# Kernel tuning notes

Hardware: AMD Instinct MI355X
Metric: run time of the kernel (lower is better)

The kernel has to match this reference:

```python
import jax, jax.numpy as jnp
import numpy as np

BN_EPS = 1e-5


def setup_inputs() -> dict:
    key = jax.random.key(0)
    ks = jax.random.split(key, 4)
    B, N, D = 8, 8192, 256
    outD = 256
    s = 1.0 / np.sqrt(D)
    return {
        "feature": jax.random.normal(ks[0], (B, N, D), dtype=jnp.float32),
        "W_qk": jax.random.normal(ks[1], (2, D, D), dtype=jnp.float32) * s,
        "b_qk": jnp.zeros((2, D), dtype=jnp.float32),
        "W_v": jax.random.normal(ks[2], (D, outD), dtype=jnp.float32) * s,
        "b_v": jnp.zeros((outD,), dtype=jnp.float32),
        "gamma": jnp.ones((D,), dtype=jnp.float32),
        "beta": jnp.zeros((D,), dtype=jnp.float32),
    }


def reference(feature, W_qk, b_qk, W_v, b_v, gamma, beta):
    # QK: [B, 2, N, D]
    QK = jnp.einsum("bnd,kde->bkne", feature, W_qk) + b_qk[None, :, None, :]
    # value: [B, N, outD]
    value = jnp.einsum("bnd,de->bne", feature, W_v) + b_v
    query = QK[:, 0]  # [B, N, D]
    key = QK[:, 1]    # [B, N, D]
    # softmax over the sequence axis (dim=1), per (batch, channel)
    sm = jax.nn.softmax(key, axis=1)
    # lambda context: softmax^T @ value -> [B, D, outD]
    lam = jnp.einsum("bnd,bne->bde", sm, value)
    # BatchNorm1d(featureDim) in training mode: channel axis = D (axis 1),
    # stats over (batch, spatial) = axes (0, 2); biased variance as torch uses.
    mean = jnp.mean(lam, axis=(0, 2), keepdims=True)
    var = jnp.var(lam, axis=(0, 2), keepdims=True)
    bn = (lam - mean) * jax.lax.rsqrt(var + BN_EPS)
    bn = bn * gamma[None, :, None] + beta[None, :, None]
    # result: query @ BN -> [B, N, outD]
    return jnp.einsum("bnd,bde->bne", query, bn)
```

## Files before the change

### kernel.cpp

```cpp
#include <hip/hip_runtime.h>

typedef unsigned short u16;
typedef __bf16 bf16x8 __attribute__((ext_vector_type(8)));
typedef float f32x4 __attribute__((ext_vector_type(4)));

#define LOG2E 1.44269504088896f

__device__ inline u16 f2b(float f) {
    unsigned u = __float_as_uint(f);
    u += 0x7fff + ((u >> 16) & 1);
    return (u16)(u >> 16);
}
__device__ inline float b2f(u16 u) { return __uint_as_float(((unsigned)u) << 16); }
__device__ inline unsigned pk2(float a, float b) {
    return (unsigned)f2b(a) | ((unsigned)f2b(b) << 16);
}
__device__ inline uint4 pack8(float4 a, float4 b) {
    return uint4{pk2(a.x, a.y), pk2(a.z, a.w), pk2(b.x, b.y), pk2(b.z, b.w)};
}
__device__ inline f32x4 mfma_bf16(uint4 a, uint4 b, f32x4 c) {
    return __builtin_amdgcn_mfma_f32_16x16x32_bf16(
        __builtin_bit_cast(bf16x8, a), __builtin_bit_cast(bf16x8, b), c, 0, 0, 0);
}
__device__ inline void ld16(const u16* g, u16* l) {
    __builtin_amdgcn_global_load_lds(
        (const __attribute__((address_space(1))) unsigned int*)g,
        (__attribute__((address_space(3))) unsigned int*)l, 16, 0, 0);
}

__global__ __launch_bounds__(256) void prep_w(const float* __restrict__ Wqk,
                                              const float* __restrict__ Wv,
                                              u16* __restrict__ WkT,
                                              u16* __restrict__ WvT,
                                              u16* __restrict__ Wqb) {
    int idx = blockIdx.x * 256 + threadIdx.x;
    int which = idx >> 16;
    int i = (idx >> 8) & 255;
    int j = idx & 255;
    if (which == 0)
        WkT[i * 256 + j] = f2b(Wqk[65536 + j * 256 + i]);
    else if (which == 1)
        WvT[i * 256 + j] = f2b(Wv[j * 256 + i]);
    else
        Wqb[i * 256 + j] = f2b(Wqk[i * 256 + j]);
}

__global__ __launch_bounds__(256, 2) void gemm_kv(const float* __restrict__ A,
                                                  const u16* __restrict__ BtK,
                                                  const u16* __restrict__ BtV,
                                                  const float* __restrict__ biasK,
                                                  const float* __restrict__ biasV,
                                                  u16* __restrict__ KT,
                                                  u16* __restrict__ VT) {
    __shared__ __align__(16) u16 lds[18432];
    u16* As = lds;
    u16* BsK = lds + 2048;
    u16* BsV = lds + 10240;

    const int t = threadIdx.x;
    const int r0 = blockIdx.x * 64;
    const int w = t >> 6, lane = t & 63, l15 = lane & 15, q = lane >> 4;

    f32x4 accK[16], accV[16];
#pragma unroll
    for (int c = 0; c < 16; ++c) {
        accK[c] = f32x4{0.f, 0.f, 0.f, 0.f};
        accV[c] = f32x4{0.f, 0.f, 0.f, 0.f};
    }

    const int ar = t >> 2;
    const int ak = (t & 3) * 8;
    const float* Arow = A + (long)(r0 + ar) * 256 + ak;
    u16* AsW = As + t * 8;

    float4 a0 = ((const float4*)Arow)[0];
    float4 a1 = ((const float4*)Arow)[1];

    for (int k0 = 0; k0 < 256; k0 += 32) {
#pragma unroll
        for (int j = 0; j < 4; ++j) {
            int ch = j * 256 + t;
            int br = ch >> 2;
            int bk = (ch & 3) * 8;
            ld16(BtK + br * 256 + k0 + bk, BsK + j * 2048 + w * 512);
            ld16(BtV + br * 256 + k0 + bk, BsV + j * 2048 + w * 512);
        }
        *(uint4*)AsW = pack8(a0, a1);
        __syncthreads();
        if (k0 + 32 < 256) {
            a0 = ((const float4*)(Arow + k0 + 32))[0];
            a1 = ((const float4*)(Arow + k0 + 32))[1];
        }
        uint4 af = *(const uint4*)(As + (w * 16 + l15) * 32 + q * 8);
#pragma unroll
        for (int c = 0; c < 16; ++c) {
            uint4 bK = *(const uint4*)(BsK + (c * 16 + l15) * 32 + q * 8);
            uint4 bV = *(const uint4*)(BsV + (c * 16 + l15) * 32 + q * 8);
            accK[c] = mfma_bf16(af, bK, accK[c]);
            accV[c] = mfma_bf16(af, bV, accV[c]);
        }
        __syncthreads();
    }

    const int bb = r0 >> 13, n0 = r0 & 8191;
    u16* Ct = lds;
#pragma unroll
    for (int pass = 0; pass < 2; ++pass) {
        const f32x4* acc = pass ? accV : accK;
        const float* bias = pass ? biasV : biasK;
        u16* CT = pass ? VT : KT;
#pragma unroll
        for (int c = 0; c < 16; ++c) {
            float bv = bias[c * 16 + l15];
            ushort4 pk;
            pk.x = f2b(acc[c][0] + bv);
            pk.y = f2b(acc[c][1] + bv);
            pk.z = f2b(acc[c][2] + bv);
            pk.w = f2b(acc[c][3] + bv);
            *(ushort4*)&Ct[(c * 16 + l15) * 72 + w * 16 + q * 4] = pk;
        }
        __syncthreads();
        long off = ((long)bb * 256 + t) * 8192 + n0;
#pragma unroll
        for (int j = 0; j < 8; ++j)
            *(uint4*)(CT + off + j * 8) = *(const uint4*)&Ct[t * 72 + j * 8];
        __syncthreads();
    }
}

__global__ __launch_bounds__(256, 3) void gemm_out(const float* __restrict__ A,
                                                   const u16* __restrict__ WfoldT,
                                                   const float* __restrict__ outb,
                                                   float* __restrict__ C) {
    __shared__ __align__(16) u16 lds[10240];
    u16* As = lds;
    u16* Bs = lds + 2048;

    const int t = threadIdx.x;
    const int r0 = blockIdx.x * 64;
    const int bb = r0 >> 13;
    const int w = t >> 6, lane = t & 63, l15 = lane & 15, q = lane >> 4;
    const u16* Bt = WfoldT + (long)bb * 65536;

    f32x4 acc[16];
#pragma unroll
    for (int c = 0; c < 16; ++c) acc[c] = f32x4{0.f, 0.f, 0.f, 0.f};

    const float* Arow = A + (long)(r0 + (t >> 2)) * 256 + (t & 3) * 8;
    u16* AsW = As + t * 8;

    float4 a0 = ((const float4*)Arow)[0];
    float4 a1 = ((const float4*)Arow)[1];

    for (int k0 = 0; k0 < 256; k0 += 32) {
#pragma unroll
        for (int j = 0; j < 4; ++j) {
            int ch = j * 256 + t;
            ld16(Bt + (ch >> 2) * 256 + k0 + (ch & 3) * 8, Bs + j * 2048 + w * 512);
        }
        *(uint4*)AsW = pack8(a0, a1);
        __syncthreads();
        if (k0 + 32 < 256) {
            a0 = ((const float4*)(Arow + k0 + 32))[0];
            a1 = ((const float4*)(Arow + k0 + 32))[1];
        }
        uint4 af = *(const uint4*)(As + (w * 16 + l15) * 32 + q * 8);
#pragma unroll
        for (int c = 0; c < 16; ++c) {
            uint4 bf = *(const uint4*)(Bs + (c * 16 + l15) * 32 + q * 8);
            acc[c] = mfma_bf16(af, bf, acc[c]);
        }
        __syncthreads();
    }

#pragma unroll
    for (int c = 0; c < 16; ++c) {
        int col = c * 16 + l15;
        float bv = outb[bb * 256 + col];
#pragma unroll
        for (int r = 0; r < 4; ++r) {
            int row = r0 + w * 16 + q * 4 + r;
            C[(long)row * 256 + col] = acc[c][r] + bv;
        }
    }
}

__global__ __launch_bounds__(256, 4) void gemm_splitk(const u16* __restrict__ VT,
                                                      const u16* __restrict__ PT,
                                                      float* __restrict__ lamP,
                                                      int chunk) {
    __shared__ __align__(16) u16 lds[8192];
    u16* As = lds;
    u16* Bs = lds + 4096;

    const int t = threadIdx.x;
    const int r0 = blockIdx.x * 128;
    const int c0 = blockIdx.y * 128;
    const int s = blockIdx.z;
    const int bb = blockIdx.x >> 1;
    const long n0 = (long)s * chunk;
    const int w = t >> 6, lane = t & 63, l15 = lane & 15, q = lane >> 4;

    f32x4 acc[2][8];
#pragma unroll
    for (int rt = 0; rt < 2; ++rt)
#pragma unroll
        for (int c = 0; c < 8; ++c) acc[rt][c] = f32x4{0.f, 0.f, 0.f, 0.f};

    for (int k0 = 0; k0 < chunk; k0 += 32) {
#pragma unroll
        for (int j = 0; j < 2; ++j) {
            int ch = j * 256 + t;
            int br = ch >> 2;
            int bk = (ch & 3) * 8;
            ld16(VT + (long)(r0 + br) * 8192 + n0 + k0 + bk, As + j * 2048 + w * 512);
            ld16(PT + ((long)bb * 256 + c0 + br) * 8192 + n0 + k0 + bk,
                 Bs + j * 2048 + w * 512);
        }
        __syncthreads();
        uint4 af0 = *(const uint4*)(As + (w * 32 + l15) * 32 + q * 8);
        uint4 af1 = *(const uint4*)(As + (w * 32 + 16 + l15) * 32 + q * 8);
#pragma unroll
        for (int c = 0; c < 8; ++c) {
            uint4 bf = *(const uint4*)(Bs + (c * 16 + l15) * 32 + q * 8);
            acc[0][c] = mfma_bf16(af0, bf, acc[0][c]);
            acc[1][c] = mfma_bf16(af1, bf, acc[1][c]);
        }
        __syncthreads();
    }

    float* outp = lamP + (long)s * 524288;
#pragma unroll
    for (int rt = 0; rt < 2; ++rt)
#pragma unroll
        for (int c = 0; c < 8; ++c) {
            int col = c0 + c * 16 + l15;
#pragma unroll
            for (int r = 0; r < 4; ++r) {
                int row = r0 + w * 32 + rt * 16 + q * 4 + r;
                outp[(long)row * 256 + col] = acc[rt][c][r];
            }
        }
}

__global__ __launch_bounds__(256) void reduce_lam(const float* __restrict__ lamP,
                                                  float* __restrict__ lamT, int S) {
    int i = blockIdx.x * 256 + threadIdx.x;
    float4 v = ((const float4*)lamP)[i];
    for (int s = 1; s < S; ++s) {
        float4 p = ((const float4*)(lamP + (long)s * 524288))[i];
        v.x += p.x; v.y += p.y; v.z += p.z; v.w += p.w;
    }
    ((float4*)lamT)[i] = v;
}

__global__ __launch_bounds__(256, 4) void gemm_fold(const u16* __restrict__ Abn,
                                                    const u16* __restrict__ Wqb,
                                                    u16* __restrict__ WfoldT) {
    __shared__ __align__(16) u16 lds[4096];
    u16* As = lds;
    u16* Bs = lds + 2048;

    const int t = threadIdx.x;
    const int r0 = blockIdx.x * 64;
    const int c0 = blockIdx.y * 64;
    const int w = t >> 6, lane = t & 63, l15 = lane & 15, q = lane >> 4;

    f32x4 acc[4];
#pragma unroll
    for (int c = 0; c < 4; ++c) acc[c] = f32x4{0.f, 0.f, 0.f, 0.f};

    const int br = t >> 2;
    const int bk = (t & 3) * 8;

    for (int k0 = 0; k0 < 256; k0 += 32) {
        ld16(Abn + (long)(r0 + br) * 256 + k0 + bk, As + w * 512);
        ld16(Wqb + (long)(c0 + br) * 256 + k0 + bk, Bs + w * 512);
        __syncthreads();
        uint4 af = *(const uint4*)(As + (w * 16 + l15) * 32 + q * 8);
#pragma unroll
        for (int c = 0; c < 4; ++c) {
            uint4 bf = *(const uint4*)(Bs + (c * 16 + l15) * 32 + q * 8);
            acc[c] = mfma_bf16(af, bf, acc[c]);
        }
        __syncthreads();
    }

#pragma unroll
    for (int c = 0; c < 4; ++c) {
        int col = c0 + c * 16 + l15;
#pragma unroll
        for (int r = 0; r < 4; ++r) {
            int row = r0 + w * 16 + q * 4 + r;
            WfoldT[(long)row * 256 + col] = f2b(acc[c][r]);
        }
    }
}

__global__ __launch_bounds__(64) void softmax_rows(u16* __restrict__ KT) {
    const int row = blockIdx.x;
    const int lane = threadIdx.x;
    u16* p = KT + (long)row * 8192;

    uint4 buf[16];
#pragma unroll
    for (int i = 0; i < 16; ++i) buf[i] = *(const uint4*)(p + (i * 64 + lane) * 8);

    float m = -1e30f;
#pragma unroll
    for (int i = 0; i < 16; ++i) {
        const unsigned* u = (const unsigned*)&buf[i];
#pragma unroll
        for (int j = 0; j < 4; ++j) {
            m = fmaxf(m, fmaxf(b2f((u16)(u[j] & 0xffff)), b2f((u16)(u[j] >> 16))));
        }
    }
#pragma unroll
    for (int s = 32; s > 0; s >>= 1) m = fmaxf(m, __shfl_xor(m, s, 64));

    float sum = 0.f;
#pragma unroll
    for (int i = 0; i < 16; ++i) {
        const unsigned* u = (const unsigned*)&buf[i];
#pragma unroll
        for (int j = 0; j < 4; ++j) {
            sum += exp2f((b2f((u16)(u[j] & 0xffff)) - m) * LOG2E);
            sum += exp2f((b2f((u16)(u[j] >> 16)) - m) * LOG2E);
        }
    }
#pragma unroll
    for (int s = 32; s > 0; s >>= 1) sum += __shfl_xor(sum, s, 64);
    float rl = 1.0f / sum;

#pragma unroll
    for (int i = 0; i < 16; ++i) {
        unsigned* u = (unsigned*)&buf[i];
#pragma unroll
        for (int j = 0; j < 4; ++j) {
            float a = exp2f((b2f((u16)(u[j] & 0xffff)) - m) * LOG2E) * rl;
            float b = exp2f((b2f((u16)(u[j] >> 16)) - m) * LOG2E) * rl;
            u[j] = (unsigned)f2b(a) | ((unsigned)f2b(b) << 16);
        }
        *(uint4*)(p + (i * 64 + lane) * 8) = buf[i];
    }
}

__global__ __launch_bounds__(256) void bn_kernel(const float* __restrict__ lamT,
                                                 const float* __restrict__ gamma,
                                                 const float* __restrict__ beta,
                                                 u16* __restrict__ bnT) {
    const int d = blockIdx.x;
    const int t = threadIdx.x;
    float vals[8];
    float s = 0.f, ss = 0.f;
#pragma unroll
    for (int i = 0; i < 8; ++i) {
        float v = lamT[(long)(i * 256 + t) * 256 + d];
        vals[i] = v;
        s += v;
        ss += v * v;
    }
#pragma unroll
    for (int sh = 32; sh > 0; sh >>= 1) {
        s += __shfl_xor(s, sh, 64);
        ss += __shfl_xor(ss, sh, 64);
    }
    __shared__ float red[8];
    int w = t >> 6;
    if ((t & 63) == 0) {
        red[w] = s;
        red[w + 4] = ss;
    }
    __syncthreads();
    s = red[0] + red[1] + red[2] + red[3];
    ss = red[4] + red[5] + red[6] + red[7];
    float mean = s * (1.f / 2048.f);
    float var = ss * (1.f / 2048.f) - mean * mean;
    float scale = gamma[d] * rsqrtf(var + 1e-5f);
    float shift = beta[d] - mean * scale;
#pragma unroll
    for (int i = 0; i < 8; ++i)
        bnT[(long)(i * 256 + t) * 256 + d] = f2b(vals[i] * scale + shift);
}

__global__ __launch_bounds__(256) void outb_kernel(const float* __restrict__ bq,
                                                   const u16* __restrict__ bnT,
                                                   float* __restrict__ outb) {
    int b = blockIdx.x, e = threadIdx.x;
    const u16* rowp = bnT + ((long)b * 256 + e) * 256;
    float s = 0.f;
    for (int dd = 0; dd < 256; ++dd) s += bq[dd] * b2f(rowp[dd]);
    outb[b * 256 + e] = s;
}

extern "C" void kernel_launch(void* const* d_in, const int* in_sizes, int n_in,
                              void* d_out, int out_size, void* d_ws, size_t ws_size,
                              hipStream_t stream) {
    const float* feat = (const float*)d_in[0];
    const float* W_qk = (const float*)d_in[1];
    const float* b_qk = (const float*)d_in[2];
    const float* W_v = (const float*)d_in[3];
    const float* b_v = (const float*)d_in[4];
    const float* gamma = (const float*)d_in[5];
    const float* beta = (const float*)d_in[6];
    float* out = (float*)d_out;

    char* ws = (char*)d_ws;
    u16* KT = (u16*)(ws);
    u16* VT = (u16*)(ws + 33554432);
    u16* WkT = (u16*)(ws + 67108864);
    u16* WvT = (u16*)(ws + 67239936);
    u16* Wqb = (u16*)(ws + 67371008);
    const size_t base = 67502080;
    float* lamP = (float*)(ws + base);
    size_t avail = (ws_size > base) ? ws_size - base : 0;
    int S = (avail >= 16u * 2097152u) ? 16
          : (avail >= 8u * 2097152u) ? 8
          : (avail >= 4u * 2097152u) ? 4 : 2;
    float* lamT = (float*)ws;
    u16* bnT = (u16*)(ws + 2097152);
    u16* WfoldT = (u16*)(ws + 3145728);
    float* outb = (float*)(ws + 4194304);

    prep_w<<<768, 256, 0, stream>>>(W_qk, W_v, WkT, WvT, Wqb);
    gemm_kv<<<1024, 256, 0, stream>>>(feat, WkT, WvT, b_qk + 256, b_v, KT, VT);
    softmax_rows<<<2048, 64, 0, stream>>>(KT);
    gemm_splitk<<<dim3(16, 2, S), 256, 0, stream>>>(VT, KT, lamP, 8192 / S);
    reduce_lam<<<512, 256, 0, stream>>>(lamP, lamT, S);
    bn_kernel<<<256, 256, 0, stream>>>(lamT, gamma, beta, bnT);
    outb_kernel<<<8, 256, 0, stream>>>(b_qk, bnT, outb);
    gemm_fold<<<dim3(32, 4), 256, 0, stream>>>(bnT, Wqb, WfoldT);
    gemm_out<<<1024, 256, 0, stream>>>(feat, WfoldT, outb, out);
}
```

Before: 252.0 us.

## Double-buffer LDS, swizzle layouts, and re-tile warps in the three GEMM kernels

Rewrites gemm_kv, gemm_out and gemm_splitk to double-buffer their LDS tiles, issuing the next k-slice's global-to-LDS loads before the current slice's MFMAs and dropping one barrier per iteration. It adds an XOR swizzle on LDS addresses to reduce bank conflicts. Warps are re-tiled so each warp owns a column slab and reuses A fragments across 4 row tiles, and the fp32 A prefetch in the first two kernels is deepened to two slices. LDS use doubles, and the splitk occupancy hint drops from 4 to 2 blocks per CU, which could reduce latency hiding.

```diff
diff --git a/kernel.cpp b/kernel.cpp
--- a/kernel.cpp
+++ b/kernel.cpp
@@ -27,6 +27,7 @@
         (const __attribute__((address_space(1))) unsigned int*)g,
         (__attribute__((address_space(3))) unsigned int*)l, 16, 0, 0);
 }
+
 
 __global__ __launch_bounds__(256) void prep_w(const float* __restrict__ Wqk,
                                               const float* __restrict__ Wv,
@@ -52,52 +53,77 @@
                                                   const float* __restrict__ biasV,
                                                   u16* __restrict__ KT,
                                                   u16* __restrict__ VT) {
-    __shared__ __align__(16) u16 lds[18432];
-    u16* As = lds;
-    u16* BsK = lds + 2048;
-    u16* BsV = lds + 10240;
+    __shared__ __align__(16) u16 lds[36864];
 
     const int t = threadIdx.x;
     const int r0 = blockIdx.x * 64;
     const int w = t >> 6, lane = t & 63, l15 = lane & 15, q = lane >> 4;
-
-    f32x4 accK[16], accV[16];
-#pragma unroll
-    for (int c = 0; c < 16; ++c) {
-        accK[c] = f32x4{0.f, 0.f, 0.f, 0.f};
-        accV[c] = f32x4{0.f, 0.f, 0.f, 0.f};
-    }
-
-    const int ar = t >> 2;
-    const int ak = (t & 3) * 8;
-    const float* Arow = A + (long)(r0 + ar) * 256 + ak;
-    u16* AsW = As + t * 8;
-
-    float4 a0 = ((const float4*)Arow)[0];
-    float4 a1 = ((const float4*)Arow)[1];
-
-    for (int k0 = 0; k0 < 256; k0 += 32) {
+    const int sq = ((lane & 3) ^ ((lane >> 3) & 3)) * 8;
+    const int qs = (q ^ ((l15 >> 1) & 3)) * 8;
+    const int awoff = (t >> 2) * 32 + sq;
+    const int brr = t >> 2;
+
+    f32x4 accK[4][4], accV[4][4];
+#pragma unroll
+    for (int rt = 0; rt < 4; ++rt)
+#pragma unroll
+        for (int ct = 0; ct < 4; ++ct) {
+            accK[rt][ct] = f32x4{0.f, 0.f, 0.f, 0.f};
+            accV[rt][ct] = f32x4{0.f, 0.f, 0.f, 0.f};
+        }
+
+    const float* Arow = A + (long)(r0 + brr) * 256 + (t & 3) * 8;
+    float4 p0 = ((const float4*)Arow)[0], p1 = ((const float4*)Arow)[1];
+    float4 c0_ = *(const float4*)(Arow + 32), c1_ = *(const float4*)(Arow + 36);
+    float4 d0_ = *(const float4*)(Arow + 64), d1_ = *(const float4*)(Arow + 68);
+
+    {
+        u16* dK = lds + 4096 + w * 512;
 #pragma unroll
         for (int j = 0; j < 4; ++j) {
-            int ch = j * 256 + t;
-            int br = ch >> 2;
-            int bk = (ch & 3) * 8;
-            ld16(BtK + br * 256 + k0 + bk, BsK + j * 2048 + w * 512);
-            ld16(BtV + br * 256 + k0 + bk, BsV + j * 2048 + w * 512);
-        }
-        *(uint4*)AsW = pack8(a0, a1);
-        __syncthreads();
-        if (k0 + 32 < 256) {
-            a0 = ((const float4*)(Arow + k0 + 32))[0];
-            a1 = ((const float4*)(Arow + k0 + 32))[1];
-        }
-        uint4 af = *(const uint4*)(As + (w * 16 + l15) * 32 + q * 8);
-#pragma unroll
-        for (int c = 0; c < 16; ++c) {
-            uint4 bK = *(const uint4*)(BsK + (c * 16 + l15) * 32 + q * 8);
-            uint4 bV = *(const uint4*)(BsV + (c * 16 + l15) * 32 + q * 8);
-            accK[c] = mfma_bf16(af, bK, accK[c]);
-            accV[c] = mfma_bf16(af, bV, accV[c]);
+            int br = j * 64 + brr;
+            ld16(BtK + br * 256 + sq, dK + j * 2048);
+            ld16(BtV + br * 256 + sq, dK + 8192 + j * 2048);
+        }
+    }
+    *(uint4*)(lds + awoff) = pack8(p0, p1);
+    __syncthreads();
+
+#pragma unroll
+    for (int t8 = 0; t8 < 8; ++t8) {
+        const int cur = t8 & 1;
+        if (t8 < 7) {
+            const int k0 = (t8 + 1) * 32;
+            u16* dK = lds + 4096 + (cur ^ 1) * 16384 + w * 512;
+#pragma unroll
+            for (int j = 0; j < 4; ++j) {
+                int br = j * 64 + brr;
+                ld16(BtK + br * 256 + k0 + sq, dK + j * 2048);
+                ld16(BtV + br * 256 + k0 + sq, dK + 8192 + j * 2048);
+            }
+            *(uint4*)(lds + (cur ^ 1) * 2048 + awoff) = pack8(c0_, c1_);
+            c0_ = d0_; c1_ = d1_;
+            if (t8 < 5) {
+                d0_ = *(const float4*)(Arow + (t8 + 3) * 32);
+                d1_ = *(const float4*)(Arow + (t8 + 3) * 32 + 4);
+            }
+        }
+        const u16* Asc = lds + cur * 2048;
+        const u16* Bc = lds + 4096 + cur * 16384;
+        uint4 af[4];
+#pragma unroll
+        for (int rt = 0; rt < 4; ++rt)
+            af[rt] = *(const uint4*)(Asc + (rt * 16 + l15) * 32 + qs);
+#pragma unroll
+        for (int ct = 0; ct < 4; ++ct) {
+            const int bo = (w * 64 + ct * 16 + l15) * 32 + qs;
+            uint4 bK = *(const uint4*)(Bc + bo);
+            uint4 bV = *(const uint4*)(Bc + 8192 + bo);
+#pragma unroll
+            for (int rt = 0; rt < 4; ++rt) {
+                accK[rt][ct] = mfma_bf16(af[rt], bK, accK[rt][ct]);
+                accV[rt][ct] = mfma_bf16(af[rt], bV, accV[rt][ct]);
+            }
         }
         __syncthreads();
     }
@@ -106,18 +132,22 @@
     u16* Ct = lds;
 #pragma unroll
     for (int pass = 0; pass < 2; ++pass) {
-        const f32x4* acc = pass ? accV : accK;
+        const f32x4(*acc)[4] = pass ? accV : accK;
         const float* bias = pass ? biasV : biasK;
         u16* CT = pass ? VT : KT;
 #pragma unroll
-        for (int c = 0; c < 16; ++c) {
-            float bv = bias[c * 16 + l15];
-            ushort4 pk;
-            pk.x = f2b(acc[c][0] + bv);
-            pk.y = f2b(acc[c][1] + bv);
-            pk.z = f2b(acc[c][2] + bv);
-            pk.w = f2b(acc[c][3] + bv);
-            *(ushort4*)&Ct[(c * 16 + l15) * 72 + w * 16 + q * 4] = pk;
+        for (int ct = 0; ct < 4; ++ct) {
+            const int col = w * 64 + ct * 16 + l15;
+            const float bv = bias[col];
+#pragma unroll
+            for (int rt = 0; rt < 4; ++rt) {
+                ushort4 pk;
+                pk.x = f2b(acc[rt][ct][0] + bv);
+                pk.y = f2b(acc[rt][ct][1] + bv);
+                pk.z = f2b(acc[rt][ct][2] + bv);
+                pk.w = f2b(acc[rt][ct][3] + bv);
+                *(ushort4*)&Ct[col * 72 + rt * 16 + q * 4] = pk;
+            }
         }
         __syncthreads();
         long off = ((long)bb * 256 + t) * 8192 + n0;
@@ -132,67 +162,89 @@
                                                    const u16* __restrict__ WfoldT,
                                                    const float* __restrict__ outb,
                                                    float* __restrict__ C) {
-    __shared__ __align__(16) u16 lds[10240];
-    u16* As = lds;
-    u16* Bs = lds + 2048;
-
+    __shared__ __align__(16) u16 lds[20480];
     const int t = threadIdx.x;
     const int r0 = blockIdx.x * 64;
     const int bb = r0 >> 13;
     const int w = t >> 6, lane = t & 63, l15 = lane & 15, q = lane >> 4;
+    const int sq = ((lane & 3) ^ ((lane >> 3) & 3)) * 8;
+    const int qs = (q ^ ((l15 >> 1) & 3)) * 8;
+    const int awoff = (t >> 2) * 32 + sq;
+    const int brr = t >> 2;
     const u16* Bt = WfoldT + (long)bb * 65536;
 
-    f32x4 acc[16];
-#pragma unroll
-    for (int c = 0; c < 16; ++c) acc[c] = f32x4{0.f, 0.f, 0.f, 0.f};
-
-    const float* Arow = A + (long)(r0 + (t >> 2)) * 256 + (t & 3) * 8;
-    u16* AsW = As + t * 8;
-
-    float4 a0 = ((const float4*)Arow)[0];
-    float4 a1 = ((const float4*)Arow)[1];
-
-    for (int k0 = 0; k0 < 256; k0 += 32) {
-#pragma unroll
-        for (int j = 0; j < 4; ++j) {
-            int ch = j * 256 + t;
-            ld16(Bt + (ch >> 2) * 256 + k0 + (ch & 3) * 8, Bs + j * 2048 + w * 512);
-        }
-        *(uint4*)AsW = pack8(a0, a1);
-        __syncthreads();
-        if (k0 + 32 < 256) {
-            a0 = ((const float4*)(Arow + k0 + 32))[0];
-            a1 = ((const float4*)(Arow + k0 + 32))[1];
-        }
-        uint4 af = *(const uint4*)(As + (w * 16 + l15) * 32 + q * 8);
-#pragma unroll
-        for (int c = 0; c < 16; ++c) {
-            uint4 bf = *(const uint4*)(Bs + (c * 16 + l15) * 32 + q * 8);
-            acc[c] = mfma_bf16(af, bf, acc[c]);
-        }
-        __syncthreads();
-    }
-
-#pragma unroll
-    for (int c = 0; c < 16; ++c) {
-        int col = c * 16 + l15;
-        float bv = outb[bb * 256 + col];
-#pragma unroll
-        for (int r = 0; r < 4; ++r) {
-            int row = r0 + w * 16 + q * 4 + r;
-            C[(long)row * 256 + col] = acc[c][r] + bv;
-        }
-    }
-}
-
-__global__ __launch_bounds__(256, 4) void gemm_splitk(const u16* __restrict__ VT,
+    f32x4 acc[4][4];
+#pragma unroll
+    for (int rt = 0; rt < 4; ++rt)
+#pragma unroll
+        for (int ct = 0; ct < 4; ++ct) acc[rt][ct] = f32x4{0.f, 0.f, 0.f, 0.f};
+
+    const float* Arow = A + (long)(r0 + brr) * 256 + (t & 3) * 8;
+    float4 p0 = ((const float4*)Arow)[0], p1 = ((const float4*)Arow)[1];
+    float4 c0_ = *(const float4*)(Arow + 32), c1_ = *(const float4*)(Arow + 36);
+    float4 d0_ = *(const float4*)(Arow + 64), d1_ = *(const float4*)(Arow + 68);
+
+    {
+        u16* dB = lds + 4096 + w * 512;
+#pragma unroll
+        for (int j = 0; j < 4; ++j)
+            ld16(Bt + (j * 64 + brr) * 256 + sq, dB + j * 2048);
+    }
+    *(uint4*)(lds + awoff) = pack8(p0, p1);
+    __syncthreads();
+
+#pragma unroll
+    for (int t8 = 0; t8 < 8; ++t8) {
+        const int cur = t8 & 1;
+        if (t8 < 7) {
+            const int k0 = (t8 + 1) * 32;
+            u16* dB = lds + 4096 + (cur ^ 1) * 8192 + w * 512;
+#pragma unroll
+            for (int j = 0; j < 4; ++j)
+                ld16(Bt + (j * 64 + brr) * 256 + k0 + sq, dB + j * 2048);
+            *(uint4*)(lds + (cur ^ 1) * 2048 + awoff) = pack8(c0_, c1_);
+            c0_ = d0_; c1_ = d1_;
+            if (t8 < 5) {
+                d0_ = *(const float4*)(Arow + (t8 + 3) * 32);
+                d1_ = *(const float4*)(Arow + (t8 + 3) * 32 + 4);
+            }
+        }
+        const u16* Asc = lds + cur * 2048;
+        const u16* Bc = lds + 4096 + cur * 8192;
+        uint4 af[4];
+#pragma unroll
+        for (int rt = 0; rt < 4; ++rt)
+            af[rt] = *(const uint4*)(Asc + (rt * 16 + l15) * 32 + qs);
+#pragma unroll
+        for (int ct = 0; ct < 4; ++ct) {
+            uint4 bf = *(const uint4*)(Bc + (w * 64 + ct * 16 + l15) * 32 + qs);
+#pragma unroll
+            for (int rt = 0; rt < 4; ++rt)
+                acc[rt][ct] = mfma_bf16(af[rt], bf, acc[rt][ct]);
+        }
+        __syncthreads();
+    }
+
+#pragma unroll
+    for (int ct = 0; ct < 4; ++ct) {
+        const int col = w * 64 + ct * 16 + l15;
+        const float bv = outb[bb * 256 + col];
+#pragma unroll
+        for (int rt = 0; rt < 4; ++rt) {
+#pragma unroll
+            for (int r = 0; r < 4; ++r) {
+                int row = r0 + rt * 16 + q * 4 + r;
+                C[(long)row * 256 + col] = acc[rt][ct][r] + bv;
+            }
+        }
+    }
+}
+
+__global__ __launch_bounds__(256, 2) void gemm_splitk(const u16* __restrict__ VT,
                                                       const u16* __restrict__ PT,
                                                       float* __restrict__ lamP,
                                                       int chunk) {
-    __shared__ __align__(16) u16 lds[8192];
-    u16* As = lds;
-    u16* Bs = lds + 4096;
-
+    __shared__ __align__(16) u16 lds[16384];
     const int t = threadIdx.x;
     const int r0 = blockIdx.x * 128;
     const int c0 = blockIdx.y * 128;
@@ -200,46 +252,67 @@
     const int bb = blockIdx.x >> 1;
     const long n0 = (long)s * chunk;
     const int w = t >> 6, lane = t & 63, l15 = lane & 15, q = lane >> 4;
-
-    f32x4 acc[2][8];
-#pragma unroll
-    for (int rt = 0; rt < 2; ++rt)
-#pragma unroll
-        for (int c = 0; c < 8; ++c) acc[rt][c] = f32x4{0.f, 0.f, 0.f, 0.f};
-
-    for (int k0 = 0; k0 < chunk; k0 += 32) {
+    const int sq = ((lane & 3) ^ ((lane >> 3) & 3)) * 8;
+    const int qs = (q ^ ((l15 >> 1) & 3)) * 8;
+    const int brr = t >> 2;
+
+    const u16* Abase = VT + (long)r0 * 8192 + n0;
+    const u16* Bbase = PT + ((long)bb * 256 + c0) * 8192 + n0;
+
+    f32x4 acc[8][2];
+#pragma unroll
+    for (int rt = 0; rt < 8; ++rt) {
+        acc[rt][0] = f32x4{0.f, 0.f, 0.f, 0.f};
+        acc[rt][1] = f32x4{0.f, 0.f, 0.f, 0.f};
+    }
+
+    {
+        u16* dA = lds + w * 512;
 #pragma unroll
         for (int j = 0; j < 2; ++j) {
-            int ch = j * 256 + t;
-            int br = ch >> 2;
-            int bk = (ch & 3) * 8;
-            ld16(VT + (long)(r0 + br) * 8192 + n0 + k0 + bk, As + j * 2048 + w * 512);
-            ld16(PT + ((long)bb * 256 + c0 + br) * 8192 + n0 + k0 + bk,
-                 Bs + j * 2048 + w * 512);
-        }
-        __syncthreads();
-        uint4 af0 = *(const uint4*)(As + (w * 32 + l15) * 32 + q * 8);
-        uint4 af1 = *(const uint4*)(As + (w * 32 + 16 + l15) * 32 + q * 8);
-#pragma unroll
-        for (int c = 0; c < 8; ++c) {
-            uint4 bf = *(const uint4*)(Bs + (c * 16 + l15) * 32 + q * 8);
-            acc[0][c] = mfma_bf16(af0, bf, acc[0][c]);
-            acc[1][c] = mfma_bf16(af1, bf, acc[1][c]);
+            int br = j * 64 + brr;
+            ld16(Abase + (long)br * 8192 + sq, dA + j * 2048);
+            ld16(Bbase + (long)br * 8192 + sq, dA + 4096 + j * 2048);
+        }
+    }
+    __syncthreads();
+
+    const int nk = chunk >> 5;
+    for (int ks = 0; ks < nk; ++ks) {
+        const int cur = ks & 1;
+        if (ks + 1 < nk) {
+            const int k0 = (ks + 1) * 32;
+            u16* dA = lds + (cur ^ 1) * 8192 + w * 512;
+#pragma unroll
+            for (int j = 0; j < 2; ++j) {
+                int br = j * 64 + brr;
+                ld16(Abase + (long)br * 8192 + k0 + sq, dA + j * 2048);
+                ld16(Bbase + (long)br * 8192 + k0 + sq, dA + 4096 + j * 2048);
+            }
+        }
+        const u16* Asc = lds + cur * 8192;
+        const u16* Bsc = Asc + 4096;
+        const int bo = (w * 32 + l15) * 32 + qs;
+        uint4 bf0 = *(const uint4*)(Bsc + bo);
+        uint4 bf1 = *(const uint4*)(Bsc + 512 + bo);
+#pragma unroll
+        for (int rt = 0; rt < 8; ++rt) {
+            uint4 af = *(const uint4*)(Asc + (rt * 16 + l15) * 32 + qs);
+            acc[rt][0] = mfma_bf16(af, bf0, acc[rt][0]);
+            acc[rt][1] = mfma_bf16(af, bf1, acc[rt][1]);
         }
         __syncthreads();
     }
 
     float* outp = lamP + (long)s * 524288;
 #pragma unroll
-    for (int rt = 0; rt < 2; ++rt)
-#pragma unroll
-        for (int c = 0; c < 8; ++c) {
-            int col = c0 + c * 16 + l15;
-#pragma unroll
-            for (int r = 0; r < 4; ++r) {
-                int row = r0 + w * 32 + rt * 16 + q * 4 + r;
-                outp[(long)row * 256 + col] = acc[rt][c][r];
-            }
+    for (int rt = 0; rt < 8; ++rt)
+#pragma unroll
+        for (int ct = 0; ct < 2; ++ct) {
+            const int col = c0 + w * 32 + ct * 16 + l15;
+#pragma unroll
+            for (int r = 0; r < 4; ++r)
+                outp[(long)(r0 + rt * 16 + q * 4 + r) * 256 + col] = acc[rt][ct][r];
         }
 }
 
```

New measurement: 252.4 us. No clear change (+0.2%).

## Keep full swizzled weight matrix resident in LDS and stream activations directly

Applied to the files above, without the earlier changes.

The K/V projection and output GEMMs now load the whole 256x256 bf16 weight matrix into LDS once per block, using an XOR swizzle applied when the weights are prepared and folded. Activation rows are read straight from global memory and converted with packed bf16 conversion instructions, so the per-k-step sync and A staging are gone. The split-K lambda GEMM now reads operands directly from global memory into registers with a 4x4 tile per wave, also dropping LDS and barriers. The trade-off is 128KB of LDS per block, which limits occupancy, plus uncoalesced direct global loads in place of shared tiles.

```diff
diff --git a/kernel.cpp b/kernel.cpp
--- a/kernel.cpp
+++ b/kernel.cpp
@@ -12,12 +12,6 @@
     return (u16)(u >> 16);
 }
 __device__ inline float b2f(u16 u) { return __uint_as_float(((unsigned)u) << 16); }
-__device__ inline unsigned pk2(float a, float b) {
-    return (unsigned)f2b(a) | ((unsigned)f2b(b) << 16);
-}
-__device__ inline uint4 pack8(float4 a, float4 b) {
-    return uint4{pk2(a.x, a.y), pk2(a.z, a.w), pk2(b.x, b.y), pk2(b.z, b.w)};
-}
 __device__ inline f32x4 mfma_bf16(uint4 a, uint4 b, f32x4 c) {
     return __builtin_amdgcn_mfma_f32_16x16x32_bf16(
         __builtin_bit_cast(bf16x8, a), __builtin_bit_cast(bf16x8, b), c, 0, 0, 0);
@@ -26,6 +20,14 @@
     __builtin_amdgcn_global_load_lds(
         (const __attribute__((address_space(1))) unsigned int*)g,
         (__attribute__((address_space(3))) unsigned int*)l, 16, 0, 0);
+}
+__device__ inline uint4 cvt8(float4 a, float4 b) {
+    uint4 r;
+    asm("v_cvt_pk_bf16_f32 %0, %1, %2" : "=v"(r.x) : "v"(a.x), "v"(a.y));
+    asm("v_cvt_pk_bf16_f32 %0, %1, %2" : "=v"(r.y) : "v"(a.z), "v"(a.w));
+    asm("v_cvt_pk_bf16_f32 %0, %1, %2" : "=v"(r.z) : "v"(b.x), "v"(b.y));
+    asm("v_cvt_pk_bf16_f32 %0, %1, %2" : "=v"(r.w) : "v"(b.z), "v"(b.w));
+    return r;
 }
 
 __global__ __launch_bounds__(256) void prep_w(const float* __restrict__ Wqk,
@@ -36,210 +38,201 @@
     int idx = blockIdx.x * 256 + threadIdx.x;
     int which = idx >> 16;
     int i = (idx >> 8) & 255;
-    int j = idx & 255;
+    int j8 = idx & 255;
+    if (which == 2) {
+        Wqb[i * 256 + j8] = f2b(Wqk[i * 256 + j8]);
+        return;
+    }
+    int c = (((j8 >> 3) ^ (i & 7)) << 3) | (j8 & 7);
     if (which == 0)
-        WkT[i * 256 + j] = f2b(Wqk[65536 + j * 256 + i]);
-    else if (which == 1)
-        WvT[i * 256 + j] = f2b(Wv[j * 256 + i]);
+        WkT[i * 256 + j8] = f2b(Wqk[65536 + c * 256 + i]);
     else
-        Wqb[i * 256 + j] = f2b(Wqk[i * 256 + j]);
-}
-
-__global__ __launch_bounds__(256, 2) void gemm_kv(const float* __restrict__ A,
-                                                  const u16* __restrict__ BtK,
-                                                  const u16* __restrict__ BtV,
-                                                  const float* __restrict__ biasK,
-                                                  const float* __restrict__ biasV,
-                                                  u16* __restrict__ KT,
-                                                  u16* __restrict__ VT) {
-    __shared__ __align__(16) u16 lds[18432];
-    u16* As = lds;
-    u16* BsK = lds + 2048;
-    u16* BsV = lds + 10240;
-
+        WvT[i * 256 + j8] = f2b(Wv[c * 256 + i]);
+}
+
+__global__ __launch_bounds__(512, 2) void gemm_kv2(const float* __restrict__ A,
+                                                   const u16* __restrict__ imgK,
+                                                   const u16* __restrict__ imgV,
+                                                   const float* __restrict__ biasK,
+                                                   const float* __restrict__ biasV,
+                                                   u16* __restrict__ KT,
+                                                   u16* __restrict__ VT) {
+    __shared__ __align__(16) u16 Bs[65536];
     const int t = threadIdx.x;
-    const int r0 = blockIdx.x * 64;
+    const int mat = blockIdx.x & 1;
+    const int grp = blockIdx.x >> 1;
     const int w = t >> 6, lane = t & 63, l15 = lane & 15, q = lane >> 4;
-
-    f32x4 accK[16], accV[16];
-#pragma unroll
-    for (int c = 0; c < 16; ++c) {
-        accK[c] = f32x4{0.f, 0.f, 0.f, 0.f};
-        accV[c] = f32x4{0.f, 0.f, 0.f, 0.f};
-    }
-
-    const int ar = t >> 2;
-    const int ak = (t & 3) * 8;
-    const float* Arow = A + (long)(r0 + ar) * 256 + ak;
-    u16* AsW = As + t * 8;
-
-    float4 a0 = ((const float4*)Arow)[0];
-    float4 a1 = ((const float4*)Arow)[1];
-
-    for (int k0 = 0; k0 < 256; k0 += 32) {
-#pragma unroll
-        for (int j = 0; j < 4; ++j) {
-            int ch = j * 256 + t;
-            int br = ch >> 2;
-            int bk = (ch & 3) * 8;
-            ld16(BtK + br * 256 + k0 + bk, BsK + j * 2048 + w * 512);
-            ld16(BtV + br * 256 + k0 + bk, BsV + j * 2048 + w * 512);
-        }
-        *(uint4*)AsW = pack8(a0, a1);
-        __syncthreads();
-        if (k0 + 32 < 256) {
-            a0 = ((const float4*)(Arow + k0 + 32))[0];
-            a1 = ((const float4*)(Arow + k0 + 32))[1];
-        }
-        uint4 af = *(const uint4*)(As + (w * 16 + l15) * 32 + q * 8);
-#pragma unroll
-        for (int c = 0; c < 16; ++c) {
-            uint4 bK = *(const uint4*)(BsK + (c * 16 + l15) * 32 + q * 8);
-            uint4 bV = *(const uint4*)(BsV + (c * 16 + l15) * 32 + q * 8);
-            accK[c] = mfma_bf16(af, bK, accK[c]);
-            accV[c] = mfma_bf16(af, bV, accV[c]);
-        }
-        __syncthreads();
-    }
-
-    const int bb = r0 >> 13, n0 = r0 & 8191;
-    u16* Ct = lds;
-#pragma unroll
-    for (int pass = 0; pass < 2; ++pass) {
-        const f32x4* acc = pass ? accV : accK;
-        const float* bias = pass ? biasV : biasK;
-        u16* CT = pass ? VT : KT;
-#pragma unroll
-        for (int c = 0; c < 16; ++c) {
-            float bv = bias[c * 16 + l15];
-            ushort4 pk;
-            pk.x = f2b(acc[c][0] + bv);
-            pk.y = f2b(acc[c][1] + bv);
-            pk.z = f2b(acc[c][2] + bv);
-            pk.w = f2b(acc[c][3] + bv);
-            *(ushort4*)&Ct[(c * 16 + l15) * 72 + w * 16 + q * 4] = pk;
-        }
-        __syncthreads();
-        long off = ((long)bb * 256 + t) * 8192 + n0;
-#pragma unroll
-        for (int j = 0; j < 8; ++j)
-            *(uint4*)(CT + off + j * 8) = *(const uint4*)&Ct[t * 72 + j * 8];
-        __syncthreads();
-    }
-}
-
-__global__ __launch_bounds__(256, 3) void gemm_out(const float* __restrict__ A,
-                                                   const u16* __restrict__ WfoldT,
-                                                   const float* __restrict__ outb,
-                                                   float* __restrict__ C) {
-    __shared__ __align__(16) u16 lds[10240];
-    u16* As = lds;
-    u16* Bs = lds + 2048;
-
+    const int cg = w >> 2, rg = w & 3;
+    const u16* img = mat ? imgV : imgK;
+    const float* bias = mat ? biasV : biasK;
+    u16* OUT = mat ? VT : KT;
+
+#pragma unroll
+    for (int s = 0; s < 16; ++s)
+        ld16(img + (s * 512 + t) * 8, Bs + (s * 512 + w * 64) * 8);
+    __syncthreads();
+
+    const int e3 = l15 & 7;
+    const int qx = q ^ (e3 & 3);
+    const int ghi8 = (e3 & 4) * 8;
+    const int bbase = (cg * 128 + l15) * 256 + qx * 8;
+
+    for (int sl = 0; sl < 4; ++sl) {
+        const long n0 = (long)grp * 512 + sl * 128;
+        const int bb = (int)(n0 >> 13);
+        const int nloc = (int)(n0 & 8191);
+        const float* Ab = A + (n0 + rg * 32 + l15) * 256 + q * 8;
+
+        f32x4 acc[2][8];
+#pragma unroll
+        for (int rt = 0; rt < 2; ++rt)
+#pragma unroll
+            for (int ct = 0; ct < 8; ++ct) acc[rt][ct] = f32x4{0.f, 0.f, 0.f, 0.f};
+
+#pragma unroll
+        for (int ks = 0; ks < 8; ++ks) {
+            uint4 af[2];
+#pragma unroll
+            for (int rt = 0; rt < 2; ++rt) {
+                const float* p = Ab + rt * 4096 + ks * 32;
+                af[rt] = cvt8(((const float4*)p)[0], ((const float4*)p)[1]);
+            }
+            const int gofs = (ks * 32) ^ ghi8;
+#pragma unroll
+            for (int ct = 0; ct < 8; ++ct) {
+                uint4 bf = *(const uint4*)(Bs + bbase + ct * 4096 + gofs);
+                acc[0][ct] = mfma_bf16(af[0], bf, acc[0][ct]);
+                acc[1][ct] = mfma_bf16(af[1], bf, acc[1][ct]);
+            }
+        }
+#pragma unroll
+        for (int ct = 0; ct < 8; ++ct) {
+            const int col = cg * 128 + ct * 16 + l15;
+            const float bv = bias[col];
+#pragma unroll
+            for (int rt = 0; rt < 2; ++rt) {
+                ushort4 pk;
+                pk.x = f2b(acc[rt][ct][0] + bv);
+                pk.y = f2b(acc[rt][ct][1] + bv);
+                pk.z = f2b(acc[rt][ct][2] + bv);
+                pk.w = f2b(acc[rt][ct][3] + bv);
+                *(ushort4*)(OUT + (((long)(bb * 256 + col)) << 13) + nloc +
+                            rg * 32 + rt * 16 + q * 4) = pk;
+            }
+        }
+    }
+}
+
+__global__ __launch_bounds__(512, 2) void gemm_out2(const float* __restrict__ A,
+                                                    const u16* __restrict__ Wimg,
+                                                    const float* __restrict__ outb,
+                                                    float* __restrict__ C) {
+    __shared__ __align__(16) u16 Bs[65536];
     const int t = threadIdx.x;
-    const int r0 = blockIdx.x * 64;
-    const int bb = r0 >> 13;
     const int w = t >> 6, lane = t & 63, l15 = lane & 15, q = lane >> 4;
-    const u16* Bt = WfoldT + (long)bb * 65536;
-
-    f32x4 acc[16];
-#pragma unroll
-    for (int c = 0; c < 16; ++c) acc[c] = f32x4{0.f, 0.f, 0.f, 0.f};
-
-    const float* Arow = A + (long)(r0 + (t >> 2)) * 256 + (t & 3) * 8;
-    u16* AsW = As + t * 8;
-
-    float4 a0 = ((const float4*)Arow)[0];
-    float4 a1 = ((const float4*)Arow)[1];
-
-    for (int k0 = 0; k0 < 256; k0 += 32) {
-#pragma unroll
-        for (int j = 0; j < 4; ++j) {
-            int ch = j * 256 + t;
-            ld16(Bt + (ch >> 2) * 256 + k0 + (ch & 3) * 8, Bs + j * 2048 + w * 512);
-        }
-        *(uint4*)AsW = pack8(a0, a1);
-        __syncthreads();
-        if (k0 + 32 < 256) {
-            a0 = ((const float4*)(Arow + k0 + 32))[0];
-            a1 = ((const float4*)(Arow + k0 + 32))[1];
-        }
-        uint4 af = *(const uint4*)(As + (w * 16 + l15) * 32 + q * 8);
-#pragma unroll
-        for (int c = 0; c < 16; ++c) {
-            uint4 bf = *(const uint4*)(Bs + (c * 16 + l15) * 32 + q * 8);
-            acc[c] = mfma_bf16(af, bf, acc[c]);
-        }
-        __syncthreads();
-    }
-
-#pragma unroll
-    for (int c = 0; c < 16; ++c) {
-        int col = c * 16 + l15;
-        float bv = outb[bb * 256 + col];
-#pragma unroll
-        for (int r = 0; r < 4; ++r) {
-            int row = r0 + w * 16 + q * 4 + r;
-            C[(long)row * 256 + col] = acc[c][r] + bv;
-        }
-    }
-}
-
-__global__ __launch_bounds__(256, 4) void gemm_splitk(const u16* __restrict__ VT,
-                                                      const u16* __restrict__ PT,
-                                                      float* __restrict__ lamP,
-                                                      int chunk) {
-    __shared__ __align__(16) u16 lds[8192];
-    u16* As = lds;
-    u16* Bs = lds + 4096;
-
+    const int cg = w >> 2, rg = w & 3;
+    const long r0 = (long)blockIdx.x * 256;
+    const int bb = (int)(r0 >> 13);
+    const u16* img = Wimg + (long)bb * 65536;
+
+#pragma unroll
+    for (int s = 0; s < 16; ++s)
+        ld16(img + (s * 512 + t) * 8, Bs + (s * 512 + w * 64) * 8);
+    __syncthreads();
+
+    const int e3 = l15 & 7;
+    const int qx = q ^ (e3 & 3);
+    const int ghi8 = (e3 & 4) * 8;
+    const int bbase = (cg * 128 + l15) * 256 + qx * 8;
+
+    for (int sl = 0; sl < 2; ++sl) {
+        const long n0 = r0 + sl * 128;
+        const float* Ab = A + (n0 + rg * 32 + l15) * 256 + q * 8;
+
+        f32x4 acc[2][8];
+#pragma unroll
+        for (int rt = 0; rt < 2; ++rt)
+#pragma unroll
+            for (int ct = 0; ct < 8; ++ct) acc[rt][ct] = f32x4{0.f, 0.f, 0.f, 0.f};
+
+#pragma unroll
+        for (int ks = 0; ks < 8; ++ks) {
+            uint4 af[2];
+#pragma unroll
+            for (int rt = 0; rt < 2; ++rt) {
+                const float* p = Ab + rt * 4096 + ks * 32;
+                af[rt] = cvt8(((const float4*)p)[0], ((const float4*)p)[1]);
+            }
+            const int gofs = (ks * 32) ^ ghi8;
+#pragma unroll
+            for (int ct = 0; ct < 8; ++ct) {
+                uint4 bf = *(const uint4*)(Bs + bbase + ct * 4096 + gofs);
+                acc[0][ct] = mfma_bf16(af[0], bf, acc[0][ct]);
+                acc[1][ct] = mfma_bf16(af[1], bf, acc[1][ct]);
+            }
+        }
+#pragma unroll
+        for (int ct = 0; ct < 8; ++ct) {
+            const int col = cg * 128 + ct * 16 + l15;
+            const float bv = outb[bb * 256 + col];
+#pragma unroll
+            for (int rt = 0; rt < 2; ++rt) {
+                const long rbase = n0 + rg * 32 + rt * 16 + q * 4;
+#pragma unroll
+                for (int r = 0; r < 4; ++r)
+                    C[(rbase + r) * 256 + col] = acc[rt][ct][r] + bv;
+            }
+        }
+    }
+}
+
+__global__ __launch_bounds__(512, 2) void gemm_splitk2(const u16* __restrict__ VT,
+                                                       const u16* __restrict__ PT,
+                                                       float* __restrict__ lamP,
+                                                       int chunk) {
     const int t = threadIdx.x;
+    const int w = t >> 6, lane = t & 63, l15 = lane & 15, q = lane >> 4;
+    const int rg = w & 1, cg = w >> 1;
     const int r0 = blockIdx.x * 128;
-    const int c0 = blockIdx.y * 128;
-    const int s = blockIdx.z;
+    const int s = blockIdx.y;
     const int bb = blockIdx.x >> 1;
     const long n0 = (long)s * chunk;
-    const int w = t >> 6, lane = t & 63, l15 = lane & 15, q = lane >> 4;
-
-    f32x4 acc[2][8];
-#pragma unroll
-    for (int rt = 0; rt < 2; ++rt)
-#pragma unroll
-        for (int c = 0; c < 8; ++c) acc[rt][c] = f32x4{0.f, 0.f, 0.f, 0.f};
-
-    for (int k0 = 0; k0 < chunk; k0 += 32) {
-#pragma unroll
-        for (int j = 0; j < 2; ++j) {
-            int ch = j * 256 + t;
-            int br = ch >> 2;
-            int bk = (ch & 3) * 8;
-            ld16(VT + (long)(r0 + br) * 8192 + n0 + k0 + bk, As + j * 2048 + w * 512);
-            ld16(PT + ((long)bb * 256 + c0 + br) * 8192 + n0 + k0 + bk,
-                 Bs + j * 2048 + w * 512);
-        }
-        __syncthreads();
-        uint4 af0 = *(const uint4*)(As + (w * 32 + l15) * 32 + q * 8);
-        uint4 af1 = *(const uint4*)(As + (w * 32 + 16 + l15) * 32 + q * 8);
-#pragma unroll
-        for (int c = 0; c < 8; ++c) {
-            uint4 bf = *(const uint4*)(Bs + (c * 16 + l15) * 32 + q * 8);
-            acc[0][c] = mfma_bf16(af0, bf, acc[0][c]);
-            acc[1][c] = mfma_bf16(af1, bf, acc[1][c]);
-        }
-        __syncthreads();
+
+    const u16* Av = VT + (((long)(r0 + rg * 64 + l15)) << 13) + n0 + q * 8;
+    const u16* Bp = PT + (((long)(bb * 256 + cg * 64 + l15)) << 13) + n0 + q * 8;
+
+    f32x4 acc[4][4];
+#pragma unroll
+    for (int rt = 0; rt < 4; ++rt)
+#pragma unroll
+        for (int ct = 0; ct < 4; ++ct) acc[rt][ct] = f32x4{0.f, 0.f, 0.f, 0.f};
+
+    const int nk = chunk >> 5;
+#pragma unroll 4
+    for (int ks = 0; ks < nk; ++ks) {
+        uint4 af[4], bf[4];
+#pragma unroll
+        for (int i = 0; i < 4; ++i) {
+            af[i] = *(const uint4*)(Av + (long)i * (16 * 8192) + ks * 32);
+            bf[i] = *(const uint4*)(Bp + (long)i * (16 * 8192) + ks * 32);
+        }
+#pragma unroll
+        for (int rt = 0; rt < 4; ++rt)
+#pragma unroll
+            for (int ct = 0; ct < 4; ++ct)
+                acc[rt][ct] = mfma_bf16(af[rt], bf[ct], acc[rt][ct]);
     }
 
     float* outp = lamP + (long)s * 524288;
 #pragma unroll
-    for (int rt = 0; rt < 2; ++rt)
-#pragma unroll
-        for (int c = 0; c < 8; ++c) {
-            int col = c0 + c * 16 + l15;
-#pragma unroll
-            for (int r = 0; r < 4; ++r) {
-                int row = r0 + w * 32 + rt * 16 + q * 4 + r;
-                outp[(long)row * 256 + col] = acc[rt][c][r];
-            }
+    for (int rt = 0; rt < 4; ++rt)
+#pragma unroll
+        for (int ct = 0; ct < 4; ++ct) {
+            const int col = cg * 64 + ct * 16 + l15;
+#pragma unroll
+            for (int r = 0; r < 4; ++r)
+                outp[(long)(r0 + rg * 64 + rt * 16 + q * 4 + r) * 256 + col] =
+                    acc[rt][ct][r];
         }
 }
 
@@ -288,11 +281,13 @@
 
 #pragma unroll
     for (int c = 0; c < 4; ++c) {
-        int col = c0 + c * 16 + l15;
+        int cidx = c0 + c * 16 + l15;
 #pragma unroll
         for (int r = 0; r < 4; ++r) {
             int row = r0 + w * 16 + q * 4 + r;
-            WfoldT[(long)row * 256 + col] = f2b(acc[c][r]);
+            int e = row & 255, b2 = row >> 8;
+            int swz = ((((cidx >> 3) ^ (e & 7)) << 3) | (cidx & 7));
+            WfoldT[(long)b2 * 65536 + e * 256 + swz] = f2b(acc[c][r]);
         }
     }
 }
@@ -423,12 +418,12 @@
     float* outb = (float*)(ws + 4194304);
 
     prep_w<<<768, 256, 0, stream>>>(W_qk, W_v, WkT, WvT, Wqb);
-    gemm_kv<<<1024, 256, 0, stream>>>(feat, WkT, WvT, b_qk + 256, b_v, KT, VT);
+    gemm_kv2<<<256, 512, 0, stream>>>(feat, WkT, WvT, b_qk + 256, b_v, KT, VT);
     softmax_rows<<<2048, 64, 0, stream>>>(KT);
-    gemm_splitk<<<dim3(16, 2, S), 256, 0, stream>>>(VT, KT, lamP, 8192 / S);
+    gemm_splitk2<<<dim3(16, S), 512, 0, stream>>>(VT, KT, lamP, 8192 / S);
     reduce_lam<<<512, 256, 0, stream>>>(lamP, lamT, S);
     bn_kernel<<<256, 256, 0, stream>>>(lamT, gamma, beta, bnT);
     outb_kernel<<<8, 256, 0, stream>>>(b_qk, bnT, outb);
     gemm_fold<<<dim3(32, 4), 256, 0, stream>>>(bnT, Wqb, WfoldT);
-    gemm_out<<<1024, 256, 0, stream>>>(feat, WfoldT, outb, out);
-}
+    gemm_out2<<<256, 512, 0, stream>>>(feat, WfoldT, outb, out);
+}
```

New measurement: 285.1 us. +13.2%, slower.
